# Kernel tuning notes

Measured on AMD Instinct MI355X. Metric: run time of the kernel, lower is better.

## Reference

```python
import jax, jax.numpy as jnp
import numpy as np

TAU = 0.5
BETA = 10.0
NUM_NODES = 200000
NUM_EDGES = 200000
NODE_DIM = 128
EDGE_DIM = 128
D = 16
GROUPS = {4: 12000, 8: 6000}


def setup_inputs() -> dict:
    key = jax.random.key(0)
    ks = jax.random.split(key, 8)
    inp = {
        "n": jax.random.normal(ks[0], (NUM_NODES, NODE_DIM), dtype=jnp.float32),
        "e": jax.random.normal(ks[1], (NUM_EDGES, EDGE_DIM), dtype=jnp.float32),
        "W": jax.random.normal(ks[2], (1, NODE_DIM, EDGE_DIM), dtype=jnp.float32) * 0.02,
        "b": jnp.zeros((1,), dtype=jnp.float32),
        "hypernode_k4": jax.random.randint(ks[3], (GROUPS[4],), 0, NUM_NODES),
        "hyperedge_k4": jax.random.randint(ks[4], (GROUPS[4], 4, D), 0, NUM_EDGES),
        "hypernode_k8": jax.random.randint(ks[5], (GROUPS[8],), 0, NUM_NODES),
        "hyperedge_k8": jax.random.randint(ks[6], (GROUPS[8], 8, D), 0, NUM_EDGES),
    }
    return inp


def _group_loss(n, e, W, b, node_idx, edge_idx, k):
    # node_idx: [N], edge_idx: [N, k, D]
    t = n[node_idx] @ W[0]                       # [N, E] anchor projected through bilinear weight
    ce = e[edge_idx]                             # [N, k, D, E] gathered contrast edges
    logits = jnp.einsum('ne,nkde->nkd', t, ce) + b[0]
    s = jnp.exp(jax.nn.sigmoid(logits) / TAU).sum(-1)   # [N, k] score_list
    suffix = jnp.cumsum(s[:, ::-1], axis=1)[:, ::-1]    # suffix sums s[:, j:].sum
    ratio = s[:, : k - 1] / suffix[:, : k - 1]
    return (-jnp.log(jnp.minimum(ratio, BETA))).sum(axis=1) / (k - 1)  # [N]


def reference(n, e, W, b, hypernode_k4, hyperedge_k4, hypernode_k8, hyperedge_k8):
    l4 = _group_loss(n, e, W, b, hypernode_k4, hyperedge_k4, 4)
    l8 = _group_loss(n, e, W, b, hypernode_k8, hyperedge_k8, 8)
    return jnp.concatenate([l4, l8]).mean()
```

## Files before the change

### kernel.cpp

```cpp
#include <hip/hip_runtime.h>
#include <hip/hip_bf16.h>

#define N4 12000
#define N8 6000
#define NTOT 18000
#define NBLK (NTOT / 4)
#define NK8BLK (N8 / 4)
#define NTBLK (NTOT / 16)
#define NE 200000

#if __has_builtin(__builtin_amdgcn_sdot4)
#define USE_SDOT4 1
#else
#define USE_SDOT4 0
#endif

#if __has_builtin(__builtin_amdgcn_sched_barrier)
#define SCHED_FENCE() __builtin_amdgcn_sched_barrier(0)
#else
#define SCHED_FENCE()
#endif

#define OFF_PART  256
#define PART_B    (NBLK * 4)
#define OFF_T8    ((OFF_PART + PART_B + 255) & ~255)
#define T8_B      (NTOT * 128)
#define OFF_E8    ((OFF_T8 + T8_B + 255) & ~255)
#define M_MIN     16384

#define E_SCALE   30.0f
#define T_SCALE   110.0f
#define INV_SCALE (1.0f / (E_SCALE * T_SCALE))

template<bool BF16>
__device__ __forceinline__ float loadf(const void* p, long i) {
    if constexpr (BF16) {
        unsigned short v = ((const unsigned short*)p)[i];
        return __uint_as_float(((unsigned int)v) << 16);
    } else {
        return ((const float*)p)[i];
    }
}

template<bool BF16>
__device__ __forceinline__ void loadpair(const void* p, long pairIdx, float& a, float& b) {
    if constexpr (BF16) {
        unsigned int u = ((const unsigned int*)p)[pairIdx];
        a = __uint_as_float(u << 16);
        b = __uint_as_float(u & 0xffff0000u);
    } else {
        float2 v = ((const float2*)p)[pairIdx];
        a = v.x; b = v.y;
    }
}

template<bool BF16> struct RawRow;
template<> struct RawRow<true> {
    uint4 v;
    __device__ __forceinline__ void unpack(float* o) const {
        o[0] = __uint_as_float(v.x << 16); o[1] = __uint_as_float(v.x & 0xffff0000u);
        o[2] = __uint_as_float(v.y << 16); o[3] = __uint_as_float(v.y & 0xffff0000u);
        o[4] = __uint_as_float(v.z << 16); o[5] = __uint_as_float(v.z & 0xffff0000u);
        o[6] = __uint_as_float(v.w << 16); o[7] = __uint_as_float(v.w & 0xffff0000u);
    }
};
template<> struct RawRow<false> {
    float4 a, b;
    __device__ __forceinline__ void unpack(float* o) const {
        o[0] = a.x; o[1] = a.y; o[2] = a.z; o[3] = a.w;
        o[4] = b.x; o[5] = b.y; o[6] = b.z; o[7] = b.w;
    }
};

__device__ __forceinline__ int qb(float x, float s) {
    return (int)rintf(fminf(fmaxf(x * s, -127.0f), 127.0f));
}

__device__ __forceinline__ unsigned int q4(const float* f, float s) {
    unsigned int r = 0;
#pragma unroll
    for (int q = 0; q < 4; q++)
        r |= ((unsigned int)qb(f[q], s) & 0xffu) << (8 * q);
    return r;
}

__device__ __forceinline__ int dot4i(unsigned int a, unsigned int b, int c) {
#if USE_SDOT4
    return __builtin_amdgcn_sdot4((int)a, (int)b, c, false);
#else
#pragma unroll
    for (int q = 0; q < 4; q++) {
        int av = ((int)(a << ((3 - q) * 8))) >> 24;
        int bv = ((int)(b << ((3 - q) * 8))) >> 24;
        c += av * bv;
    }
    return c;
#endif
}

__device__ __forceinline__ bool detect_bf16(const void* W) {
    const unsigned short* u = (const unsigned short*)W;
    const int lane = threadIdx.x & 63;
    bool wild = false;
#pragma unroll
    for (int q = 0; q < 4; q++) {
        float f = __uint_as_float(((unsigned int)u[lane * 4 + q]) << 16);
        if (!(fabsf(f) < 1.0f)) wild = true;
    }
    return __ballot(wild) == 0ull;
}

__device__ __forceinline__ int heavy_first(int b) {
    return (b < NK8BLK) ? (b + (N4 / 4)) : (b - NK8BLK);
}

template<bool BF16>
__device__ __forceinline__ void t4_body(int lane, float* nl, int rbase,
                                        const void* n, const void* W,
                                        const int* hn4, const int* hn8,
                                        unsigned char* t8) {
#pragma unroll
    for (int r = 0; r < 4; r++) {
        int row = rbase + r;
        int node = (row < N4) ? hn4[row] : hn8[row - N4];
        long nb = (long)node * 128;
        nl[lane * 4 + r]        = loadf<BF16>(n, nb + lane);
        nl[(lane + 64) * 4 + r] = loadf<BF16>(n, nb + 64 + lane);
    }
    float t0[4] = {0, 0, 0, 0}, t1[4] = {0, 0, 0, 0};
#pragma unroll 8
    for (int c = 0; c < 128; c++) {
        float4 nc = *(const float4*)(nl + c * 4);
        float w0, w1;
        loadpair<BF16>(W, (long)c * 64 + lane, w0, w1);
        t0[0] = fmaf(nc.x, w0, t0[0]); t1[0] = fmaf(nc.x, w1, t1[0]);
        t0[1] = fmaf(nc.y, w0, t0[1]); t1[1] = fmaf(nc.y, w1, t1[1]);
        t0[2] = fmaf(nc.z, w0, t0[2]); t1[2] = fmaf(nc.z, w1, t1[2]);
        t0[3] = fmaf(nc.w, w0, t0[3]); t1[3] = fmaf(nc.w, w1, t1[3]);
    }
#pragma unroll
    for (int r = 0; r < 4; r++) {
        int b0 = qb(t0[r], T_SCALE), b1 = qb(t1[r], T_SCALE);
        ((unsigned short*)(t8 + (long)(rbase + r) * 128))[lane] =
            (unsigned short)((b0 & 0xff) | ((b1 & 0xff) << 8));
    }
}

__global__ __launch_bounds__(256) void k_prep(
    const void* n, const void* e, const void* W,
    const int* hn4, const int* hn8,
    unsigned char* t8, uint2* e8)
{
    const bool bf = detect_bf16(W);
    if (blockIdx.x < NTBLK) {
        __shared__ __align__(16) float nl4[4][512];
        const int lane = threadIdx.x & 63, wave = threadIdx.x >> 6;
        const int rbase = (blockIdx.x * 4 + wave) * 4;
        if (bf) t4_body<true >(lane, nl4[wave], rbase, n, W, hn4, hn8, t8);
        else    t4_body<false>(lane, nl4[wave], rbase, n, W, hn4, hn8, t8);
    } else {
        long gid = (long)(blockIdx.x - NTBLK) * 256 + threadIdx.x;
        float f[8];
        if (bf) {
            RawRow<true> r; r.v = ((const uint4*)e)[gid]; r.unpack(f);
        } else {
            RawRow<false> r;
            const float4* p = ((const float4*)e) + gid * 2;
            r.a = p[0]; r.b = p[1]; r.unpack(f);
        }
        e8[gid] = make_uint2(q4(f, E_SCALE), q4(f + 4, E_SCALE));
    }
}

template<int K, bool FULL>
__device__ __forceinline__ float row_body(
    int lane, int row, const int* ebase,
    const void* e, const unsigned char* e8, const unsigned char* t8,
    long M, float bval, bool bf)
{
    const int sub = lane & 7, grp = lane >> 3;
    constexpr int NCH = K * 2;
    constexpr int PF = (NCH < 8) ? NCH : 8;

    int idx[NCH];
    {
        const int4* ip = (const int4*)(ebase + grp * NCH);
#pragma unroll
        for (int q = 0; q < NCH / 4; q++) {
            int4 v = ip[q];
            idx[4 * q] = v.x; idx[4 * q + 1] = v.y; idx[4 * q + 2] = v.z; idx[4 * q + 3] = v.w;
        }
    }

    uint4 tqv = *(const uint4*)(t8 + (long)row * 128 + sub * 16);

    uint4 buf[PF];
#pragma unroll
    for (int i = 0; i < PF; i++) {
        if (FULL || idx[i] < M)
            buf[i] = *(const uint4*)(e8 + (unsigned int)idx[i] * 128u + sub * 16);
    }
    SCHED_FENCE();

    float sacc = 0.0f;
#pragma unroll
    for (int ch = 0; ch < NCH; ch++) {
        uint4 v = buf[ch % PF];
        bool cov = FULL || (idx[ch] < M);
        if (ch + PF < NCH) {
            if (FULL || idx[ch + PF] < M)
                buf[ch % PF] = *(const uint4*)(e8 + (unsigned int)idx[ch + PF] * 128u + sub * 16);
        }
        SCHED_FENCE();

        if (!cov) {
            float ev[16];
            long eidx = idx[ch];
            if (bf) {
                RawRow<true> r0, r1;
                r0.v = *(const uint4*)(((const unsigned short*)e) + eidx * 128 + sub * 16);
                r1.v = *(const uint4*)(((const unsigned short*)e) + eidx * 128 + sub * 16 + 8);
                r0.unpack(ev); r1.unpack(ev + 8);
            } else {
                const float4* p = (const float4*)(((const float*)e) + eidx * 128 + sub * 16);
#pragma unroll
                for (int q = 0; q < 4; q++) {
                    float4 x = p[q];
                    ev[4 * q] = x.x; ev[4 * q + 1] = x.y; ev[4 * q + 2] = x.z; ev[4 * q + 3] = x.w;
                }
            }
            v.x = q4(ev, E_SCALE); v.y = q4(ev + 4, E_SCALE);
            v.z = q4(ev + 8, E_SCALE); v.w = q4(ev + 12, E_SCALE);
        }

        int d = 0;
        d = dot4i(v.x, tqv.x, d);
        d = dot4i(v.y, tqv.y, d);
        d = dot4i(v.z, tqv.z, d);
        d = dot4i(v.w, tqv.w, d);
        float dotf = (float)d * INV_SCALE;

        dotf += __shfl_xor(dotf, 1);
        dotf += __shfl_xor(dotf, 2);
        dotf += __shfl_xor(dotf, 4);

        float logit = dotf + bval;
        float sig = 1.0f / (1.0f + __expf(-logit));
        sacc += __expf(sig * 2.0f);
    }

    float s_all[K];
#pragma unroll
    for (int j = 0; j < K; j++) {
        if constexpr (K == 4) s_all[j] = __shfl(sacc, j * 16) + __shfl(sacc, j * 16 + 8);
        else                  s_all[j] = __shfl(sacc, j * 8);
    }

    float lsum = 0.0f;
    if (lane == 0) {
        float suffix = s_all[K - 1];
#pragma unroll
        for (int j = K - 2; j >= 0; j--) {
            suffix += s_all[j];
            float ratio = fminf(s_all[j] / suffix, 10.0f);
            lsum += -__logf(ratio);
        }
        lsum /= (float)(K - 1);
    }
    return lsum;
}

template<bool FULL>
__global__ __launch_bounds__(256) void k_main(
    const void* e, const unsigned char* e8, const unsigned char* t8, long M,
    const void* W, const void* bptr,
    const int* he4, const int* he8, float* part)
{
    __shared__ float wsum[4];
    const int lane = threadIdx.x & 63, wave = threadIdx.x >> 6;
    const int blk = heavy_first(blockIdx.x);
    const int row = blk * 4 + wave;
    const bool bf = detect_bf16(W);
    const float bval = bf ? loadf<true>(bptr, 0) : loadf<false>(bptr, 0);

    float lsum;
    if (row < N4) {
        lsum = row_body<4, FULL>(lane, row, he4 + (long)row * 64, e, e8, t8, M, bval, bf);
    } else {
        int r = row - N4;
        lsum = row_body<8, FULL>(lane, row, he8 + (long)r * 128, e, e8, t8, M, bval, bf);
    }
    if (lane == 0) wsum[wave] = lsum;
    __syncthreads();
    if (threadIdx.x == 0) part[blockIdx.x] = wsum[0] + wsum[1] + wsum[2] + wsum[3];
}

__global__ __launch_bounds__(256) void k_sumpart(const float* part, const void* W, void* out) {
    __shared__ float ws[4];
    const int tid = threadIdx.x;
    const bool bf = detect_bf16(W);
    float v = 0.0f;
    for (int i = tid; i < NBLK; i += 256) v += part[i];
    v += __shfl_xor(v,1); v += __shfl_xor(v,2); v += __shfl_xor(v,4);
    v += __shfl_xor(v,8); v += __shfl_xor(v,16); v += __shfl_xor(v,32);
    if ((tid & 63) == 0) ws[tid >> 6] = v;
    __syncthreads();
    if (tid == 0) {
        float m = (ws[0]+ws[1]+ws[2]+ws[3]) / (float)NTOT;
        if (bf) ((__hip_bfloat16*)out)[0] = __float2bfloat16(m);
        else    ((float*)out)[0] = m;
    }
}

extern "C" void kernel_launch(void* const* d_in, const int* in_sizes, int n_in,
                              void* d_out, int out_size, void* d_ws, size_t ws_size,
                              hipStream_t stream) {
    const void* n    = d_in[0];
    const void* e    = d_in[1];
    const void* W    = d_in[2];
    const void* bptr = d_in[3];
    const int* hn4 = (const int*)d_in[4];
    const int* he4 = (const int*)d_in[5];
    const int* hn8 = (const int*)d_in[6];
    const int* he8 = (const int*)d_in[7];

    char* ws = (char*)d_ws;
    float* part = (float*)(ws + OFF_PART);
    unsigned char* t8 = (unsigned char*)(ws + OFF_T8);
    unsigned char* e8 = (unsigned char*)(ws + OFF_E8);

    long M = 0;
    if (ws_size >= (size_t)OFF_E8 + (size_t)M_MIN * 128) {
        M = (long)((ws_size - OFF_E8) / 128);
        if (M > NE) M = NE;
        M &= ~15L;
    }

    k_prep<<<NTBLK + (int)(M / 16), 256, 0, stream>>>(n, e, W, hn4, hn8, t8, (uint2*)e8);

    if (M >= NE)
        k_main<true ><<<NBLK, 256, 0, stream>>>(e, e8, t8, (long)NE, W, bptr, he4, he8, part);
    else
        k_main<false><<<NBLK, 256, 0, stream>>>(e, e8, t8, M, W, bptr, he4, he8, part);
    k_sumpart<<<1, 256, 0, stream>>>(part, W, d_out);
}
```

Before: 252.9 us.

## Widen prep tiles, interleave projection blocks, and issue all edge loads upfront

The anchor-projection prep now computes 8 rows per wave instead of 4, so each W load is reused across twice as many rows. Projection blocks are interleaved among the edge-quantization blocks so the two kinds of work share the GPU more evenly. Each quantization thread now handles 16 values instead of 8, using wider loads and stores. In the main kernel, the rolling 8-deep prefetch is replaced by loading every chunk's quantized edge row before any compute, which raises register pressure for k=8. The interleaving assumes a large grid, so the partial-cache fallback could skip projection blocks when the workspace is small.

```diff
diff --git a/kernel.cpp b/kernel.cpp
--- a/kernel.cpp
+++ b/kernel.cpp
@@ -6,8 +6,12 @@
 #define NTOT 18000
 #define NBLK (NTOT / 4)
 #define NK8BLK (N8 / 4)
-#define NTBLK (NTOT / 16)
 #define NE 200000
+
+#define NT8BLK 563
+#define NEBLK  6250
+#define TSTRIDE 12
+#define PREP_GRID (NT8BLK + NEBLK)
 
 #if __has_builtin(__builtin_amdgcn_sdot4)
 #define USE_SDOT4 1
@@ -54,24 +58,6 @@
     }
 }
 
-template<bool BF16> struct RawRow;
-template<> struct RawRow<true> {
-    uint4 v;
-    __device__ __forceinline__ void unpack(float* o) const {
-        o[0] = __uint_as_float(v.x << 16); o[1] = __uint_as_float(v.x & 0xffff0000u);
-        o[2] = __uint_as_float(v.y << 16); o[3] = __uint_as_float(v.y & 0xffff0000u);
-        o[4] = __uint_as_float(v.z << 16); o[5] = __uint_as_float(v.z & 0xffff0000u);
-        o[6] = __uint_as_float(v.w << 16); o[7] = __uint_as_float(v.w & 0xffff0000u);
-    }
-};
-template<> struct RawRow<false> {
-    float4 a, b;
-    __device__ __forceinline__ void unpack(float* o) const {
-        o[0] = a.x; o[1] = a.y; o[2] = a.z; o[3] = a.w;
-        o[4] = b.x; o[5] = b.y; o[6] = b.z; o[7] = b.w;
-    }
-};
-
 __device__ __forceinline__ int qb(float x, float s) {
     return (int)rintf(fminf(fmaxf(x * s, -127.0f), 127.0f));
 }
@@ -115,60 +101,97 @@
 }
 
 template<bool BF16>
-__device__ __forceinline__ void t4_body(int lane, float* nl, int rbase,
+__device__ __forceinline__ void t8_body(int lane, float* nl, int rbase,
                                         const void* n, const void* W,
                                         const int* hn4, const int* hn8,
                                         unsigned char* t8) {
 #pragma unroll
-    for (int r = 0; r < 4; r++) {
+    for (int r = 0; r < 8; r++) {
         int row = rbase + r;
-        int node = (row < N4) ? hn4[row] : hn8[row - N4];
-        long nb = (long)node * 128;
-        nl[lane * 4 + r]        = loadf<BF16>(n, nb + lane);
-        nl[(lane + 64) * 4 + r] = loadf<BF16>(n, nb + 64 + lane);
-    }
-    float t0[4] = {0, 0, 0, 0}, t1[4] = {0, 0, 0, 0};
+        float v0 = 0.0f, v1 = 0.0f;
+        if (row < NTOT) {
+            int node = (row < N4) ? hn4[row] : hn8[row - N4];
+            long nb = (long)node * 128;
+            v0 = loadf<BF16>(n, nb + lane);
+            v1 = loadf<BF16>(n, nb + 64 + lane);
+        }
+        nl[lane * 8 + r]        = v0;
+        nl[(lane + 64) * 8 + r] = v1;
+    }
+    float t0[8], t1[8];
+#pragma unroll
+    for (int r = 0; r < 8; r++) { t0[r] = 0.0f; t1[r] = 0.0f; }
 #pragma unroll 8
     for (int c = 0; c < 128; c++) {
-        float4 nc = *(const float4*)(nl + c * 4);
+        float4 na = *(const float4*)(nl + c * 8);
+        float4 nb = *(const float4*)(nl + c * 8 + 4);
         float w0, w1;
         loadpair<BF16>(W, (long)c * 64 + lane, w0, w1);
-        t0[0] = fmaf(nc.x, w0, t0[0]); t1[0] = fmaf(nc.x, w1, t1[0]);
-        t0[1] = fmaf(nc.y, w0, t0[1]); t1[1] = fmaf(nc.y, w1, t1[1]);
-        t0[2] = fmaf(nc.z, w0, t0[2]); t1[2] = fmaf(nc.z, w1, t1[2]);
-        t0[3] = fmaf(nc.w, w0, t0[3]); t1[3] = fmaf(nc.w, w1, t1[3]);
-    }
-#pragma unroll
-    for (int r = 0; r < 4; r++) {
-        int b0 = qb(t0[r], T_SCALE), b1 = qb(t1[r], T_SCALE);
-        ((unsigned short*)(t8 + (long)(rbase + r) * 128))[lane] =
-            (unsigned short)((b0 & 0xff) | ((b1 & 0xff) << 8));
+        t0[0] = fmaf(na.x, w0, t0[0]); t1[0] = fmaf(na.x, w1, t1[0]);
+        t0[1] = fmaf(na.y, w0, t0[1]); t1[1] = fmaf(na.y, w1, t1[1]);
+        t0[2] = fmaf(na.z, w0, t0[2]); t1[2] = fmaf(na.z, w1, t1[2]);
+        t0[3] = fmaf(na.w, w0, t0[3]); t1[3] = fmaf(na.w, w1, t1[3]);
+        t0[4] = fmaf(nb.x, w0, t0[4]); t1[4] = fmaf(nb.x, w1, t1[4]);
+        t0[5] = fmaf(nb.y, w0, t0[5]); t1[5] = fmaf(nb.y, w1, t1[5]);
+        t0[6] = fmaf(nb.z, w0, t0[6]); t1[6] = fmaf(nb.z, w1, t1[6]);
+        t0[7] = fmaf(nb.w, w0, t0[7]); t1[7] = fmaf(nb.w, w1, t1[7]);
+    }
+#pragma unroll
+    for (int r = 0; r < 8; r++) {
+        int row = rbase + r;
+        if (row < NTOT) {
+            int b0 = qb(t0[r], T_SCALE), b1 = qb(t1[r], T_SCALE);
+            ((unsigned short*)(t8 + (long)row * 128))[lane] =
+                (unsigned short)((b0 & 0xff) | ((b1 & 0xff) << 8));
+        }
     }
 }
 
 __global__ __launch_bounds__(256) void k_prep(
     const void* n, const void* e, const void* W,
     const int* hn4, const int* hn8,
-    unsigned char* t8, uint2* e8)
+    unsigned char* t8, uint4* e8)
 {
     const bool bf = detect_bf16(W);
-    if (blockIdx.x < NTBLK) {
-        __shared__ __align__(16) float nl4[4][512];
+    const int b = blockIdx.x;
+
+    bool is_t = false;
+    int tb = 0, eb = 0;
+    if (b < NT8BLK * TSTRIDE) {
+        if (b % TSTRIDE == 0) { is_t = true; tb = b / TSTRIDE; }
+        else                  { eb = b - b / TSTRIDE - 1; }
+    } else {
+        eb = b - NT8BLK;
+    }
+
+    if (is_t) {
+        __shared__ __align__(16) float nl8[4][1024];
         const int lane = threadIdx.x & 63, wave = threadIdx.x >> 6;
-        const int rbase = (blockIdx.x * 4 + wave) * 4;
-        if (bf) t4_body<true >(lane, nl4[wave], rbase, n, W, hn4, hn8, t8);
-        else    t4_body<false>(lane, nl4[wave], rbase, n, W, hn4, hn8, t8);
-    } else {
-        long gid = (long)(blockIdx.x - NTBLK) * 256 + threadIdx.x;
-        float f[8];
+        const int rbase = (tb * 4 + wave) * 8;
+        if (bf) t8_body<true >(lane, nl8[wave], rbase, n, W, hn4, hn8, t8);
+        else    t8_body<false>(lane, nl8[wave], rbase, n, W, hn4, hn8, t8);
+    } else {
+        long gid = (long)eb * 256 + threadIdx.x;
+        float f[16];
         if (bf) {
-            RawRow<true> r; r.v = ((const uint4*)e)[gid]; r.unpack(f);
+            const uint4* p = ((const uint4*)e) + gid * 2;
+            uint4 a = p[0], bb = p[1];
+            const unsigned int w[8] = {a.x, a.y, a.z, a.w, bb.x, bb.y, bb.z, bb.w};
+#pragma unroll
+            for (int q = 0; q < 8; q++) {
+                f[2 * q]     = __uint_as_float(w[q] << 16);
+                f[2 * q + 1] = __uint_as_float(w[q] & 0xffff0000u);
+            }
         } else {
-            RawRow<false> r;
-            const float4* p = ((const float4*)e) + gid * 2;
-            r.a = p[0]; r.b = p[1]; r.unpack(f);
-        }
-        e8[gid] = make_uint2(q4(f, E_SCALE), q4(f + 4, E_SCALE));
+            const float4* p = ((const float4*)e) + gid * 4;
+#pragma unroll
+            for (int q = 0; q < 4; q++) {
+                float4 x = p[q];
+                f[4 * q] = x.x; f[4 * q + 1] = x.y; f[4 * q + 2] = x.z; f[4 * q + 3] = x.w;
+            }
+        }
+        e8[gid] = make_uint4(q4(f, E_SCALE), q4(f + 4, E_SCALE),
+                             q4(f + 8, E_SCALE), q4(f + 12, E_SCALE));
     }
 }
 
@@ -180,7 +203,6 @@
 {
     const int sub = lane & 7, grp = lane >> 3;
     constexpr int NCH = K * 2;
-    constexpr int PF = (NCH < 8) ? NCH : 8;
 
     int idx[NCH];
     {
@@ -194,9 +216,9 @@
 
     uint4 tqv = *(const uint4*)(t8 + (long)row * 128 + sub * 16);
 
-    uint4 buf[PF];
-#pragma unroll
-    for (int i = 0; i < PF; i++) {
+    uint4 buf[NCH];
+#pragma unroll
+    for (int i = 0; i < NCH; i++) {
         if (FULL || idx[i] < M)
             buf[i] = *(const uint4*)(e8 + (unsigned int)idx[i] * 128u + sub * 16);
     }
@@ -205,22 +227,19 @@
     float sacc = 0.0f;
 #pragma unroll
     for (int ch = 0; ch < NCH; ch++) {
-        uint4 v = buf[ch % PF];
-        bool cov = FULL || (idx[ch] < M);
-        if (ch + PF < NCH) {
-            if (FULL || idx[ch + PF] < M)
-                buf[ch % PF] = *(const uint4*)(e8 + (unsigned int)idx[ch + PF] * 128u + sub * 16);
-        }
-        SCHED_FENCE();
-
-        if (!cov) {
+        uint4 v = buf[ch];
+        if (!FULL && idx[ch] >= M) {
             float ev[16];
             long eidx = idx[ch];
             if (bf) {
-                RawRow<true> r0, r1;
-                r0.v = *(const uint4*)(((const unsigned short*)e) + eidx * 128 + sub * 16);
-                r1.v = *(const uint4*)(((const unsigned short*)e) + eidx * 128 + sub * 16 + 8);
-                r0.unpack(ev); r1.unpack(ev + 8);
+                const uint4* p = (const uint4*)(((const unsigned short*)e) + eidx * 128 + sub * 16);
+                uint4 a = p[0], bb = p[1];
+                const unsigned int w[8] = {a.x, a.y, a.z, a.w, bb.x, bb.y, bb.z, bb.w};
+#pragma unroll
+                for (int q = 0; q < 8; q++) {
+                    ev[2 * q]     = __uint_as_float(w[q] << 16);
+                    ev[2 * q + 1] = __uint_as_float(w[q] & 0xffff0000u);
+                }
             } else {
                 const float4* p = (const float4*)(((const float*)e) + eidx * 128 + sub * 16);
 #pragma unroll
@@ -336,11 +355,15 @@
         M &= ~15L;
     }
 
-    k_prep<<<NTBLK + (int)(M / 16), 256, 0, stream>>>(n, e, W, hn4, hn8, t8, (uint2*)e8);
-
-    if (M >= NE)
+    if (M >= NE) {
+        k_prep<<<PREP_GRID, 256, 0, stream>>>(n, e, W, hn4, hn8, t8, (uint4*)e8);
         k_main<true ><<<NBLK, 256, 0, stream>>>(e, e8, t8, (long)NE, W, bptr, he4, he8, part);
-    else
+    } else {
+        int neblk = (int)(M / 16 / 16);
+        neblk = (int)(M / 32);
+        int grid = NT8BLK + neblk;
+        k_prep<<<grid, 256, 0, stream>>>(n, e, W, hn4, hn8, t8, (uint4*)e8);
         k_main<false><<<NBLK, 256, 0, stream>>>(e, e8, t8, M, W, bptr, he4, he8, part);
+    }
     k_sumpart<<<1, 256, 0, stream>>>(part, W, d_out);
 }
```

Result: slower. 282.8 us (+11.8%).
